# Performance work log

Measured on AMD Instinct MI355X. Metric: run time of the kernel, lower is better.

Reference implementation:

```python
import jax, jax.numpy as jnp
import numpy as np

# Fixed tetrahedral (kanchor=4) rotation->anchor permutation table, taken verbatim
# from the docstring in the original source (trace_idx_ori).
TRACE_IDX_ORI = jnp.array([
    [0, 1, 2, 3], [0, 2, 3, 1], [0, 3, 1, 2],
    [1, 2, 0, 3], [1, 0, 3, 2], [1, 3, 2, 0],
    [2, 3, 0, 1], [2, 0, 1, 3], [2, 1, 3, 0],
    [3, 1, 0, 2], [3, 0, 2, 1], [3, 2, 1, 0]], dtype=jnp.int32)

B, A, N, M, D, H = 1, 4, 384, 384, 256, 8
C = D // H  # d_model_per_head = 32
NR = TRACE_IDX_ORI.shape[0]  # 12 rotations


def _project_heads(x, W, b):
    # x: (b, a, n, d) -> (b, a, h, n, c)
    y = x @ W.T + b
    bb, aa, nn, _ = y.shape
    return y.reshape(bb, aa, nn, H, C).transpose(0, 1, 3, 2, 4)


def setup_inputs() -> dict:
    key = jax.random.key(0)
    ks = jax.random.split(key, 6)
    s = 1.0 / np.sqrt(D).astype(np.float32)
    return {
        "input_q": jax.random.normal(ks[0], (B, A, N, D), dtype=jnp.float32),
        "input_k": jax.random.normal(ks[1], (B, A, M, D), dtype=jnp.float32),
        "input_v": jax.random.normal(ks[2], (B, A, M, D), dtype=jnp.float32),
        "Wq": jax.random.normal(ks[3], (D, D), dtype=jnp.float32) * s,
        "bq": jnp.zeros((D,), dtype=jnp.float32),
        "Wk": jax.random.normal(ks[4], (D, D), dtype=jnp.float32) * s,
        "bk": jnp.zeros((D,), dtype=jnp.float32),
        "Wv": jax.random.normal(ks[5], (D, D), dtype=jnp.float32) * s,
        "bv": jnp.zeros((D,), dtype=jnp.float32),
    }


def reference(input_q, input_k, input_v, Wq, bq, Wk, bk, Wv, bv):
    # Step 0: linear projections + split heads.  q,k,v: (b, a, h, n|m, c)
    q = _project_heads(input_q, Wq, bq)
    k = _project_heads(input_k, Wk, bk)
    v = _project_heads(input_v, Wv, bv)

    # Step 1: per-anchor-pair local attention scores: (b, a, e, h, n, m)
    scores_ae = jnp.einsum('bahnc,behmc->baehnm', q, k) / jnp.sqrt(
        jnp.asarray(C, dtype=q.dtype))

    # Step 2: rotation-wise gather (attn_mode='r_soft', alternative_impl=False).
    # For rotation r, query anchor a attends to key anchor trace_idx_ori[r, a]:
    # scores_rot[b, r, a] = scores_ae[b, a, trace_idx_ori[r, a]]  -> (b, nr, a, h, n, m)
    a_idx = jnp.arange(A, dtype=jnp.int32)[None, :]  # (1, A) broadcasts vs (NR, A)
    scores_rot = scores_ae[:, a_idx, TRACE_IDX_ORI]

    # Global rotation attention: pool over anchors/heads/points (attn_r_summ='mean',
    # attn_r_multihead=False), make non-negative ('sq'), normalize over rotations.
    pooled = jnp.mean(scores_rot, axis=(2, 3, 4, 5))  # (b, nr)
    pos = pooled * pooled
    attn_r = pos / jnp.sum(pos, axis=-1, keepdims=True)  # (b, nr)

    # Step 3+4: softmax over key points per rotation, gather values per rotation,
    # then weight by the global rotation attention.
    attn_local = jax.nn.softmax(scores_rot, axis=-1)  # (b, nr, a, h, n, m)
    v_rot = v[:, TRACE_IDX_ORI]  # (b, nr, a, h, m, c)
    hidden = jnp.einsum('br,brahnm,brahmc->bahnc', attn_r, attn_local, v_rot)

    # Merge heads: (b, a, h, n, c) -> (b, a, n, h*c)
    out = hidden.transpose(0, 1, 3, 2, 4).reshape(B, A, N, D)
    return out
```

## Files before the change

kernel.cpp:

```cpp
#include <hip/hip_runtime.h>
#include <hip/hip_bf16.h>

typedef __attribute__((ext_vector_type(8))) short s8x8;
typedef __attribute__((ext_vector_type(4))) float f32x4;

__device__ __forceinline__ ushort f2bf(float x) {
    union { float f; unsigned u; } c; c.f = x;
    unsigned r = c.u + 0x7FFFu + ((c.u >> 16) & 1u);
    return (ushort)(r >> 16);
}
__device__ __forceinline__ float bf2f(ushort b) {
    union { unsigned u; float f; } c; c.u = ((unsigned)b) << 16;
    return c.f;
}

__global__ __launch_bounds__(256) void proj_kernel(
    const float* __restrict__ Xq, const float* __restrict__ Xk,
    const float* __restrict__ Xv,
    const float* __restrict__ Wq, const float* __restrict__ bq,
    const float* __restrict__ Wk, const float* __restrict__ bk,
    const float* __restrict__ Wv, const float* __restrict__ bv,
    ushort* __restrict__ qh, ushort* __restrict__ ql,
    ushort* __restrict__ kh, ushort* __restrict__ kl,
    ushort* __restrict__ vh)
{
    const int z = blockIdx.z;
    const float* X    = (z == 0) ? Xq : (z == 1) ? Xk : Xv;
    const float* W    = (z == 0) ? Wq : (z == 1) ? Wk : Wv;
    const float* bias = (z == 0) ? bq : (z == 1) ? bk : bv;

    __shared__ float Xs[64][17];
    __shared__ float Ws[64][17];
    __shared__ float T[64][65];

    const int tid = threadIdx.x;
    const int row0 = blockIdx.x * 64;
    const int col0 = blockIdx.y * 64;
    const int tx = tid & 15;
    const int ty = tid >> 4;

    float acc[4][4];
    #pragma unroll
    for (int i = 0; i < 4; ++i)
        #pragma unroll
        for (int j = 0; j < 4; ++j) acc[i][j] = 0.f;

    for (int kt = 0; kt < 256; kt += 16) {
        const int r  = tid >> 2;
        const int k4 = (tid & 3) * 4;
        float4 xv = *(const float4*)&X[(row0 + r) * 256 + kt + k4];
        Xs[r][k4 + 0] = xv.x; Xs[r][k4 + 1] = xv.y;
        Xs[r][k4 + 2] = xv.z; Xs[r][k4 + 3] = xv.w;
        float4 wv = *(const float4*)&W[(col0 + r) * 256 + kt + k4];
        Ws[r][k4 + 0] = wv.x; Ws[r][k4 + 1] = wv.y;
        Ws[r][k4 + 2] = wv.z; Ws[r][k4 + 3] = wv.w;
        __syncthreads();
        #pragma unroll
        for (int kk = 0; kk < 16; ++kk) {
            float xr[4], wc[4];
            #pragma unroll
            for (int i = 0; i < 4; ++i) xr[i] = Xs[ty + 16 * i][kk];
            #pragma unroll
            for (int j = 0; j < 4; ++j) wc[j] = Ws[tx + 16 * j][kk];
            #pragma unroll
            for (int i = 0; i < 4; ++i)
                #pragma unroll
                for (int j = 0; j < 4; ++j) acc[i][j] += xr[i] * wc[j];
        }
        __syncthreads();
    }

    if (z != 2) {
        #pragma unroll
        for (int i = 0; i < 4; ++i) {
            const int row = row0 + ty + 16 * i;
            const int ae = row / 384;
            const int n = row - ae * 384;
            #pragma unroll
            for (int j = 0; j < 4; ++j) {
                const int d = col0 + tx + 16 * j;
                const int hd = d >> 5;
                const int c = d & 31;
                const float v = acc[i][j] + bias[d];
                const ushort hb = f2bf(v);
                const ushort lb = f2bf(v - bf2f(hb));
                if (z == 0) {
                    const size_t idx = ((size_t)((ae * 8 + hd) * 384 + n)) * 32 + c;
                    qh[idx] = hb; ql[idx] = lb;
                } else {
                    const size_t idx =
                        ((size_t)(((ae * 8 + hd) * 4 + (c >> 3)) * 384 + n)) * 8 + (c & 7);
                    kh[idx] = hb; kl[idx] = lb;
                }
            }
        }
    } else {
        #pragma unroll
        for (int i = 0; i < 4; ++i)
            #pragma unroll
            for (int j = 0; j < 4; ++j)
                T[ty + 16 * i][tx + 16 * j] = acc[i][j] + bias[col0 + tx + 16 * j];
        __syncthreads();
        const int cc_l = tid >> 2;
        const int nb = (tid & 3) * 16;
        const int d = col0 + cc_l;
        const int hd = d >> 5;
        const int c = d & 31;
        const int ae = row0 / 384;
        const int e8h = ae * 8 + hd;
        ushort hbuf[16] __attribute__((aligned(16)));
        #pragma unroll
        for (int k16 = 0; k16 < 16; ++k16)
            hbuf[k16] = f2bf(T[nb + k16][cc_l]);
        const size_t base = (size_t)(e8h * 32 + c) * 384 + (row0 % 384) + nb;
        *(uint4*)&vh[base] = *(const uint4*)&hbuf[0];
        *(uint4*)&vh[base + 8] = *(const uint4*)&hbuf[8];
    }
}

__global__ __launch_bounds__(192) void attn_mfma_kernel(
    const ushort* __restrict__ qhb, const ushort* __restrict__ qlb,
    const ushort* __restrict__ khb, const ushort* __restrict__ klb,
    const ushort* __restrict__ vhb,
    float* __restrict__ Sout, float* __restrict__ msum_part)
{
    __shared__ ushort Kh[4 * 192 * 8];
    __shared__ ushort Kl[4 * 192 * 8];
    __shared__ ushort Vh[32 * 200];
    __shared__ float  Pl[3][2][16][36];
    __shared__ float  red[192];

    const int strip = blockIdx.x;
    const int aeh   = blockIdx.y;
    const int hh    = aeh & 7;
    const int ee    = (aeh >> 3) & 3;
    const int aa    = aeh >> 5;
    const int e8h   = ee * 8 + hh;
    const int a8h   = aa * 8 + hh;
    const int tid   = threadIdx.x;
    const int wave  = tid >> 6;
    const int lane  = tid & 63;
    const int lg    = lane >> 4;
    const int ll    = lane & 15;

    s8x8 qfh[2], qfl[2];
    #pragma unroll
    for (int r = 0; r < 2; ++r) {
        const int n0 = strip * 96 + (2 * wave + r) * 16;
        const size_t off = (size_t)(a8h * 384 + n0 + ll) * 32 + lg * 8;
        qfh[r] = *(const s8x8*)&qhb[off];
        qfl[r] = *(const s8x8*)&qlb[off];
    }

    f32x4 oacc[2][2];
    #pragma unroll
    for (int r = 0; r < 2; ++r)
        #pragma unroll
        for (int ct = 0; ct < 2; ++ct)
            oacc[r][ct] = (f32x4){0.f, 0.f, 0.f, 0.f};
    float lsum[2][4];
    #pragma unroll
    for (int r = 0; r < 2; ++r)
        #pragma unroll
        for (int j = 0; j < 4; ++j) lsum[r][j] = 0.f;
    float rs = 0.f;
    const float sc = 0.17677669529663687f;

    for (int half = 0; half < 2; ++half) {
        #pragma unroll
        for (int i = 0; i < 4; ++i) {
            const size_t src = ((size_t)(e8h * 4 + i) * 384 + half * 192 + tid) * 8;
            *(uint4*)&Kh[(i * 192 + tid) * 8] = *(const uint4*)&khb[src];
            *(uint4*)&Kl[(i * 192 + tid) * 8] = *(const uint4*)&klb[src];
        }
        #pragma unroll
        for (int i = 0; i < 4; ++i) {
            const int u = tid + 192 * i;
            const int c = u / 24;
            const int m8 = (u - c * 24) * 8;
            *(uint4*)&Vh[c * 200 + m8] =
                *(const uint4*)&vhb[(size_t)(e8h * 32 + c) * 384 + half * 192 + m8];
        }
        __syncthreads();

        for (int mt2 = 0; mt2 < 6; ++mt2) {
            #pragma unroll
            for (int sub = 0; sub < 2; ++sub) {
                const int mt = mt2 * 2 + sub;
                const s8x8 kfh = *(const s8x8*)&Kh[(lg * 192 + mt * 16 + ll) * 8];
                const s8x8 kfl = *(const s8x8*)&Kl[(lg * 192 + mt * 16 + ll) * 8];
                #pragma unroll
                for (int r = 0; r < 2; ++r) {
                    f32x4 s = {0.f, 0.f, 0.f, 0.f};
                    s = __builtin_amdgcn_mfma_f32_16x16x32_bf16(qfh[r], kfh, s, 0, 0, 0);
                    s = __builtin_amdgcn_mfma_f32_16x16x32_bf16(qfl[r], kfh, s, 0, 0, 0);
                    s = __builtin_amdgcn_mfma_f32_16x16x32_bf16(qfh[r], kfl, s, 0, 0, 0);
                    rs += s[0] + s[1] + s[2] + s[3];
                    #pragma unroll
                    for (int j = 0; j < 4; ++j) {
                        const float p = __expf(s[j] * sc);
                        lsum[r][j] += p;
                        Pl[wave][r][lg * 4 + j][sub * 16 + ll] = p;
                    }
                }
            }
            const int mloc = mt2 * 32;
            const s8x8 vf0 = *(const s8x8*)&Vh[(0  + ll) * 200 + mloc + lg * 8];
            const s8x8 vf1 = *(const s8x8*)&Vh[(16 + ll) * 200 + mloc + lg * 8];
            #pragma unroll
            for (int r = 0; r < 2; ++r) {
                const float* prow = &Pl[wave][r][ll][lg * 8];
                s8x8 pah, pal;
                #pragma unroll
                for (int e2 = 0; e2 < 8; ++e2) {
                    const float pv = prow[e2];
                    const ushort hb = f2bf(pv);
                    pah[e2] = (short)hb;
                    pal[e2] = (short)f2bf(pv - bf2f(hb));
                }
                oacc[r][0] = __builtin_amdgcn_mfma_f32_16x16x32_bf16(pah, vf0, oacc[r][0], 0, 0, 0);
                oacc[r][0] = __builtin_amdgcn_mfma_f32_16x16x32_bf16(pal, vf0, oacc[r][0], 0, 0, 0);
                oacc[r][1] = __builtin_amdgcn_mfma_f32_16x16x32_bf16(pah, vf1, oacc[r][1], 0, 0, 0);
                oacc[r][1] = __builtin_amdgcn_mfma_f32_16x16x32_bf16(pal, vf1, oacc[r][1], 0, 0, 0);
            }
        }
        __syncthreads();
    }

    #pragma unroll
    for (int r = 0; r < 2; ++r) {
        #pragma unroll
        for (int j = 0; j < 4; ++j) {
            float L = lsum[r][j];
            L += __shfl_xor(L, 1);
            L += __shfl_xor(L, 2);
            L += __shfl_xor(L, 4);
            L += __shfl_xor(L, 8);
            const float invL = 1.f / L;
            const int row = strip * 96 + (2 * wave + r) * 16 + lg * 4 + j;
            const size_t base = (size_t)(aeh * 384 + row) * 32;
            Sout[base + 0  + ll] = oacc[r][0][j] * invL;
            Sout[base + 16 + ll] = oacc[r][1][j] * invL;
        }
    }

    red[tid] = rs * sc;
    __syncthreads();
    for (int off = 96; off >= 3; off >>= 1) {
        if (tid < off) red[tid] += red[tid + off];
        __syncthreads();
    }
    if (tid == 0) msum_part[aeh * 4 + strip] = red[0] + red[1] + red[2];
}

__global__ __launch_bounds__(256) void stats_kernel(
    const float* __restrict__ msum_part, float* __restrict__ wout)
{
    __shared__ float sh[128];
    __shared__ float cell[16];
    const int tid = threadIdx.x;
    if (tid < 128) {
        float s = 0.f;
        #pragma unroll
        for (int j = 0; j < 4; ++j) s += msum_part[tid * 4 + j];
        sh[tid] = s;
    }
    __syncthreads();
    if (tid < 16) {
        const int base = (tid >> 2) * 32 + (tid & 3) * 8;
        float s = 0.f;
        #pragma unroll
        for (int hh = 0; hh < 8; ++hh) s += sh[base + hh];
        cell[tid] = s;
    }
    __syncthreads();
    if (tid == 0) {
        const int TR[12][4] = {
            {0,1,2,3},{0,2,3,1},{0,3,1,2},{1,2,0,3},{1,0,3,2},{1,3,2,0},
            {2,3,0,1},{2,0,1,3},{2,1,3,0},{3,1,0,2},{3,0,2,1},{3,2,1,0}};
        const float denom = 4.0f * 8.0f * 384.0f * 384.0f;
        float pos[12];
        float psum = 0.f;
        for (int r = 0; r < 12; ++r) {
            float s = 0.f;
            for (int aa = 0; aa < 4; ++aa) s += cell[aa * 4 + TR[r][aa]];
            const float pooled = s / denom;
            pos[r] = pooled * pooled;
            psum += pos[r];
        }
        float w[16];
        for (int i = 0; i < 16; ++i) w[i] = 0.f;
        const float ip = 1.f / psum;
        for (int r = 0; r < 12; ++r)
            for (int aa = 0; aa < 4; ++aa) w[aa * 4 + TR[r][aa]] += pos[r] * ip;
        for (int i = 0; i < 16; ++i) wout[i] = w[i];
    }
}

__global__ __launch_bounds__(256) void combine_kernel(
    const float* __restrict__ S, const float* __restrict__ w,
    float* __restrict__ out)
{
    const int idx = blockIdx.x * 256 + threadIdx.x;
    const int a = idx / 98304;
    const int rem = idx - a * 98304;
    const int n = rem >> 8;
    const int d = rem & 255;
    const int h = d >> 5;
    const int c = d & 31;
    float r = 0.f;
    #pragma unroll
    for (int e = 0; e < 4; ++e)
        r += w[a * 4 + e] * S[(size_t)(((a * 4 + e) * 8 + h) * 384 + n) * 32 + c];
    out[idx] = r;
}

extern "C" void kernel_launch(void* const* d_in, const int* in_sizes, int n_in,
                              void* d_out, int out_size, void* d_ws, size_t ws_size,
                              hipStream_t stream)
{
    const float* in_q = (const float*)d_in[0];
    const float* in_k = (const float*)d_in[1];
    const float* in_v = (const float*)d_in[2];
    const float* Wq   = (const float*)d_in[3];
    const float* bq   = (const float*)d_in[4];
    const float* Wk   = (const float*)d_in[5];
    const float* bk   = (const float*)d_in[6];
    const float* Wv   = (const float*)d_in[7];
    const float* bv   = (const float*)d_in[8];

    const size_t NE = 393216;
    ushort* qh = (ushort*)d_ws;
    ushort* ql = qh + NE;
    ushort* kh = ql + NE;
    ushort* kl = kh + NE;
    ushort* vh = kl + NE;
    float*  Sb = (float*)((char*)d_ws + 5 * NE * sizeof(ushort));
    float*  ms = Sb + 1572864;
    float*  wb = ms + 512;
    float*  outp = (float*)d_out;

    dim3 pgrid(24, 4, 3);
    proj_kernel<<<pgrid, 256, 0, stream>>>(in_q, in_k, in_v, Wq, bq, Wk, bk,
                                           Wv, bv, qh, ql, kh, kl, vh);
    dim3 agrid(4, 128);
    attn_mfma_kernel<<<agrid, 192, 0, stream>>>(qh, ql, kh, kl, vh, Sb, ms);
    stats_kernel<<<1, 256, 0, stream>>>(ms, wb);
    combine_kernel<<<1536, 256, 0, stream>>>(Sb, wb, outp);
}
```

Before: 53.97 us.

## Rewrite projection GEMM with split-bf16 MFMA and raise MFMA wave priority

The projection kernel moves from scalar FP32 FMA tiling to bf16 MFMA. It uses a hi/lo split with three products per tile to keep close to FP32 accuracy. The weight tile is converted once into LDS in an MFMA-friendly layout, while X fragments are loaded straight from global memory and split in registers. The block shrinks to 128 threads and the V transpose epilogue is rewritten for the new fragment layout. Separately, s_setprio is placed around the MFMA groups in the attention kernel to favour the waves issuing matrix ops. The risks are extra conversion work and uncoalesced direct global loads of X.

```diff
diff --git a/kernel.cpp b/kernel.cpp
--- a/kernel.cpp
+++ b/kernel.cpp
@@ -14,7 +14,7 @@
     return c.f;
 }
 
-__global__ __launch_bounds__(256) void proj_kernel(
+__global__ __launch_bounds__(128) void proj_mfma_kernel(
     const float* __restrict__ Xq, const float* __restrict__ Xk,
     const float* __restrict__ Xv,
     const float* __restrict__ Wq, const float* __restrict__ bq,
@@ -24,97 +24,139 @@
     ushort* __restrict__ kh, ushort* __restrict__ kl,
     ushort* __restrict__ vh)
 {
+    __shared__ ushort smem[2][16384];
+
     const int z = blockIdx.z;
     const float* X    = (z == 0) ? Xq : (z == 1) ? Xk : Xv;
     const float* W    = (z == 0) ? Wq : (z == 1) ? Wk : Wv;
     const float* bias = (z == 0) ? bq : (z == 1) ? bk : bv;
 
-    __shared__ float Xs[64][17];
-    __shared__ float Ws[64][17];
-    __shared__ float T[64][65];
-
-    const int tid = threadIdx.x;
+    const int tid  = threadIdx.x;
     const int row0 = blockIdx.x * 64;
     const int col0 = blockIdx.y * 64;
-    const int tx = tid & 15;
-    const int ty = tid >> 4;
-
-    float acc[4][4];
-    #pragma unroll
-    for (int i = 0; i < 4; ++i)
-        #pragma unroll
-        for (int j = 0; j < 4; ++j) acc[i][j] = 0.f;
-
-    for (int kt = 0; kt < 256; kt += 16) {
-        const int r  = tid >> 2;
-        const int k4 = (tid & 3) * 4;
-        float4 xv = *(const float4*)&X[(row0 + r) * 256 + kt + k4];
-        Xs[r][k4 + 0] = xv.x; Xs[r][k4 + 1] = xv.y;
-        Xs[r][k4 + 2] = xv.z; Xs[r][k4 + 3] = xv.w;
-        float4 wv = *(const float4*)&W[(col0 + r) * 256 + kt + k4];
-        Ws[r][k4 + 0] = wv.x; Ws[r][k4 + 1] = wv.y;
-        Ws[r][k4 + 2] = wv.z; Ws[r][k4 + 3] = wv.w;
-        __syncthreads();
-        #pragma unroll
-        for (int kk = 0; kk < 16; ++kk) {
-            float xr[4], wc[4];
-            #pragma unroll
-            for (int i = 0; i < 4; ++i) xr[i] = Xs[ty + 16 * i][kk];
-            #pragma unroll
-            for (int j = 0; j < 4; ++j) wc[j] = Ws[tx + 16 * j][kk];
-            #pragma unroll
-            for (int i = 0; i < 4; ++i)
+
+    #pragma unroll
+    for (int i = 0; i < 32; ++i) {
+        const int idx4 = tid + 128 * i;
+        const int col  = idx4 >> 6;
+        const int k4   = (idx4 & 63) * 4;
+        const float4 wv = *(const float4*)&W[(col0 + col) * 256 + k4];
+        const int kk = k4 >> 5;
+        const int lg = (k4 >> 3) & 3;
+        const int i0 = k4 & 7;
+        const int base = ((kk * 4 + lg) * 64 + col) * 8 + i0;
+        ushort hb[4], lb[4];
+        const float w0[4] = {wv.x, wv.y, wv.z, wv.w};
+        #pragma unroll
+        for (int j = 0; j < 4; ++j) {
+            hb[j] = f2bf(w0[j]);
+            lb[j] = f2bf(w0[j] - bf2f(hb[j]));
+        }
+        *(uint2*)&smem[0][base] = *(const uint2*)&hb[0];
+        *(uint2*)&smem[1][base] = *(const uint2*)&lb[0];
+    }
+    __syncthreads();
+
+    const int wave = tid >> 6;
+    const int lane = tid & 63;
+    const int lg   = lane >> 4;
+    const int ll   = lane & 15;
+
+    f32x4 acc[2][4];
+    #pragma unroll
+    for (int r = 0; r < 2; ++r)
+        #pragma unroll
+        for (int c = 0; c < 4; ++c) acc[r][c] = (f32x4){0.f, 0.f, 0.f, 0.f};
+
+    for (int kk = 0; kk < 8; ++kk) {
+        s8x8 ah[2], al[2];
+        #pragma unroll
+        for (int rt = 0; rt < 2; ++rt) {
+            const int row = row0 + wave * 32 + rt * 16 + ll;
+            const float* xp = &X[(size_t)row * 256 + kk * 32 + lg * 8];
+            const float4 x0 = *(const float4*)&xp[0];
+            const float4 x1 = *(const float4*)&xp[4];
+            const float xv[8] = {x0.x, x0.y, x0.z, x0.w, x1.x, x1.y, x1.z, x1.w};
+            #pragma unroll
+            for (int j = 0; j < 8; ++j) {
+                const ushort hb = f2bf(xv[j]);
+                ah[rt][j] = (short)hb;
+                al[rt][j] = (short)f2bf(xv[j] - bf2f(hb));
+            }
+        }
+        #pragma unroll
+        for (int ct = 0; ct < 4; ++ct) {
+            const int boff = ((kk * 4 + lg) * 64 + ct * 16 + ll) * 8;
+            const s8x8 bh = *(const s8x8*)&smem[0][boff];
+            const s8x8 bl = *(const s8x8*)&smem[1][boff];
+            #pragma unroll
+            for (int rt = 0; rt < 2; ++rt) {
+                acc[rt][ct] = __builtin_amdgcn_mfma_f32_16x16x32_bf16(ah[rt], bh, acc[rt][ct], 0, 0, 0);
+                acc[rt][ct] = __builtin_amdgcn_mfma_f32_16x16x32_bf16(al[rt], bh, acc[rt][ct], 0, 0, 0);
+                acc[rt][ct] = __builtin_amdgcn_mfma_f32_16x16x32_bf16(ah[rt], bl, acc[rt][ct], 0, 0, 0);
+            }
+        }
+    }
+
+    float bct[4];
+    #pragma unroll
+    for (int ct = 0; ct < 4; ++ct) bct[ct] = bias[col0 + ct * 16 + ll];
+
+    if (z != 2) {
+        #pragma unroll
+        for (int rt = 0; rt < 2; ++rt) {
+            #pragma unroll
+            for (int j = 0; j < 4; ++j) {
+                const int row = row0 + wave * 32 + rt * 16 + lg * 4 + j;
+                const int ae = row / 384;
+                const int n = row - ae * 384;
                 #pragma unroll
-                for (int j = 0; j < 4; ++j) acc[i][j] += xr[i] * wc[j];
-        }
-        __syncthreads();
-    }
-
-    if (z != 2) {
-        #pragma unroll
-        for (int i = 0; i < 4; ++i) {
-            const int row = row0 + ty + 16 * i;
-            const int ae = row / 384;
-            const int n = row - ae * 384;
+                for (int ct = 0; ct < 4; ++ct) {
+                    const int d = col0 + ct * 16 + ll;
+                    const int hd = d >> 5;
+                    const int c = d & 31;
+                    const float v = acc[rt][ct][j] + bct[ct];
+                    const ushort hb = f2bf(v);
+                    const ushort lb = f2bf(v - bf2f(hb));
+                    if (z == 0) {
+                        const size_t idx = ((size_t)((ae * 8 + hd) * 384 + n)) * 32 + c;
+                        qh[idx] = hb; ql[idx] = lb;
+                    } else {
+                        const size_t idx =
+                            ((size_t)(((ae * 8 + hd) * 4 + (c >> 3)) * 384 + n)) * 8 + (c & 7);
+                        kh[idx] = hb; kl[idx] = lb;
+                    }
+                }
+            }
+        }
+    } else {
+        __syncthreads();
+        float* T = (float*)&smem[0][0];
+        #pragma unroll
+        for (int rt = 0; rt < 2; ++rt)
             #pragma unroll
             for (int j = 0; j < 4; ++j) {
-                const int d = col0 + tx + 16 * j;
-                const int hd = d >> 5;
-                const int c = d & 31;
-                const float v = acc[i][j] + bias[d];
-                const ushort hb = f2bf(v);
-                const ushort lb = f2bf(v - bf2f(hb));
-                if (z == 0) {
-                    const size_t idx = ((size_t)((ae * 8 + hd) * 384 + n)) * 32 + c;
-                    qh[idx] = hb; ql[idx] = lb;
-                } else {
-                    const size_t idx =
-                        ((size_t)(((ae * 8 + hd) * 4 + (c >> 3)) * 384 + n)) * 8 + (c & 7);
-                    kh[idx] = hb; kl[idx] = lb;
-                }
-            }
-        }
-    } else {
-        #pragma unroll
-        for (int i = 0; i < 4; ++i)
-            #pragma unroll
-            for (int j = 0; j < 4; ++j)
-                T[ty + 16 * i][tx + 16 * j] = acc[i][j] + bias[col0 + tx + 16 * j];
-        __syncthreads();
-        const int cc_l = tid >> 2;
-        const int nb = (tid & 3) * 16;
-        const int d = col0 + cc_l;
+                const int rl = wave * 32 + rt * 16 + lg * 4 + j;
+                #pragma unroll
+                for (int ct = 0; ct < 4; ++ct)
+                    T[rl * 65 + ct * 16 + ll] = acc[rt][ct][j] + bct[ct];
+            }
+        __syncthreads();
+        const int col_l = tid >> 1;
+        const int mh    = (tid & 1) * 32;
+        const int d = col0 + col_l;
         const int hd = d >> 5;
         const int c = d & 31;
-        const int ae = row0 / 384;
-        const int e8h = ae * 8 + hd;
-        ushort hbuf[16] __attribute__((aligned(16)));
-        #pragma unroll
-        for (int k16 = 0; k16 < 16; ++k16)
-            hbuf[k16] = f2bf(T[nb + k16][cc_l]);
-        const size_t base = (size_t)(e8h * 32 + c) * 384 + (row0 % 384) + nb;
-        *(uint4*)&vh[base] = *(const uint4*)&hbuf[0];
-        *(uint4*)&vh[base + 8] = *(const uint4*)&hbuf[8];
+        const int e = row0 / 384;
+        const int m0 = row0 - e * 384;
+        ushort hbuf[32] __attribute__((aligned(16)));
+        #pragma unroll
+        for (int k32 = 0; k32 < 32; ++k32)
+            hbuf[k32] = f2bf(T[(mh + k32) * 65 + col_l]);
+        const size_t base = (size_t)((e * 8 + hd) * 32 + c) * 384 + m0 + mh;
+        #pragma unroll
+        for (int u = 0; u < 4; ++u)
+            *(uint4*)&vh[base + u * 8] = *(const uint4*)&hbuf[u * 8];
     }
 }
 
@@ -192,9 +234,11 @@
                 #pragma unroll
                 for (int r = 0; r < 2; ++r) {
                     f32x4 s = {0.f, 0.f, 0.f, 0.f};
+                    __builtin_amdgcn_s_setprio(1);
                     s = __builtin_amdgcn_mfma_f32_16x16x32_bf16(qfh[r], kfh, s, 0, 0, 0);
                     s = __builtin_amdgcn_mfma_f32_16x16x32_bf16(qfl[r], kfh, s, 0, 0, 0);
                     s = __builtin_amdgcn_mfma_f32_16x16x32_bf16(qfh[r], kfl, s, 0, 0, 0);
+                    __builtin_amdgcn_s_setprio(0);
                     rs += s[0] + s[1] + s[2] + s[3];
                     #pragma unroll
                     for (int j = 0; j < 4; ++j) {
@@ -218,10 +262,12 @@
                     pah[e2] = (short)hb;
                     pal[e2] = (short)f2bf(pv - bf2f(hb));
                 }
+                __builtin_amdgcn_s_setprio(1);
                 oacc[r][0] = __builtin_amdgcn_mfma_f32_16x16x32_bf16(pah, vf0, oacc[r][0], 0, 0, 0);
                 oacc[r][0] = __builtin_amdgcn_mfma_f32_16x16x32_bf16(pal, vf0, oacc[r][0], 0, 0, 0);
                 oacc[r][1] = __builtin_amdgcn_mfma_f32_16x16x32_bf16(pah, vf1, oacc[r][1], 0, 0, 0);
                 oacc[r][1] = __builtin_amdgcn_mfma_f32_16x16x32_bf16(pal, vf1, oacc[r][1], 0, 0, 0);
+                __builtin_amdgcn_s_setprio(0);
             }
         }
         __syncthreads();
@@ -341,8 +387,8 @@
     float*  outp = (float*)d_out;
 
     dim3 pgrid(24, 4, 3);
-    proj_kernel<<<pgrid, 256, 0, stream>>>(in_q, in_k, in_v, Wq, bq, Wk, bk,
-                                           Wv, bv, qh, ql, kh, kl, vh);
+    proj_mfma_kernel<<<pgrid, 128, 0, stream>>>(in_q, in_k, in_v, Wq, bq, Wk, bk,
+                                                Wv, bv, qh, ql, kh, kl, vh);
     dim3 agrid(4, 128);
     attn_mfma_kernel<<<agrid, 192, 0, stream>>>(qh, ql, kh, kl, vh, Sb, ms);
     stats_kernel<<<1, 256, 0, stream>>>(ms, wb);
```

Measured after the change: 43.39 us. -19.6%, faster.
